# Performance work log

Hardware: AMD Instinct MI355X
Metric: run time of the kernel (lower is better)

The kernel has to match this reference:

```python
import jax, jax.numpy as jnp
import numpy as np

B, T, S, D, V, NX = 4, 256, 400, 512, 50000, 50
VEXT = V + NX  # extended vocab


def setup_inputs() -> dict:
    key = jax.random.key(0)
    ks = jax.random.split(key, 10)
    s = 0.02
    return {
        "x": jax.random.normal(ks[0], (B, T, D), dtype=jnp.float32),
        "enc_outputs": jax.random.normal(ks[1], (B, S, D), dtype=jnp.float32),
        "src_mask": jax.random.randint(ks[2], (B, 1, S), 0, 2, dtype=jnp.int32),
        "enc_batch_extend_vocab": jax.random.randint(ks[3], (B, S), 0, VEXT, dtype=jnp.int64),
        "extra_zeros": jnp.zeros((B, T, NX), dtype=jnp.float32),
        "fc_w": jax.random.normal(ks[4], (V, D), dtype=jnp.float32) * s,
        "fc_b": jnp.zeros((V,), dtype=jnp.float32),
        "pgen_w": jax.random.normal(ks[5], (1, D), dtype=jnp.float32) * s,
        "pgen_b": jnp.zeros((1,), dtype=jnp.float32),
        "wq": jax.random.normal(ks[6], (D, D), dtype=jnp.float32) * s,
        "bq": jnp.zeros((D,), dtype=jnp.float32),
        "wk": jax.random.normal(ks[7], (D, D), dtype=jnp.float32) * s,
        "bk": jnp.zeros((D,), dtype=jnp.float32),
    }


def reference(x, enc_outputs, src_mask, enc_batch_extend_vocab, extra_zeros,
              fc_w, fc_b, pgen_w, pgen_b, wq, bq, wk, bk):
    # vocab distribution: [B,T,V]
    p_vocab = jax.nn.softmax(x @ fc_w.T + fc_b, axis=-1)
    # single-head cross attention probs (h=1 -> d_k = D)
    q = x @ wq.T + bq                 # [B,T,D]
    k = enc_outputs @ wk.T + bk       # [B,S,D]
    scores = jnp.einsum('btd,bsd->bts', q, k) / jnp.sqrt(jnp.float32(D))
    scores = jnp.where(src_mask == 0, jnp.float32(-1e9), scores)  # mask [B,1,S]
    attn_probs = jax.nn.softmax(scores, axis=-1)  # [B,T,S]
    # generation gate
    p_gen = jax.nn.sigmoid(x @ pgen_w.T + pgen_b)  # [B,T,1]
    attn_dist = (1.0 - p_gen) * attn_probs         # copy distribution over source
    p_ext = jnp.concatenate([p_gen * p_vocab, extra_zeros], axis=-1)  # [B,T,VEXT]
    # scatter-add copy probs into extended vocab slots
    b_idx = jnp.arange(B)[:, None, None]
    t_idx = jnp.arange(T)[None, :, None]
    v_idx = enc_batch_extend_vocab[:, None, :]
    bb, tt, vv = jnp.broadcast_arrays(b_idx, t_idx, v_idx)  # each [B,T,S]
    p_ext = p_ext.at[bb, tt, vv].add(attn_dist)
    return jnp.log(jnp.maximum(p_ext, jnp.float32(1e-9)))
```

## Files before the change

kernel.cpp:

```cpp
#include <hip/hip_runtime.h>
#include <hip/hip_bf16.h>
#include <math.h>

constexpr int cB = 4, cT = 256, cS = 400, cD = 512, cV = 50000, cNX = 50;
constexpr int cVEXT = cV + cNX;
constexpr int cPAN  = (cV + 127) / 128;
constexpr int cCBLD = cVEXT * 2;

typedef __attribute__((ext_vector_type(8))) short short8v;
typedef __attribute__((ext_vector_type(4))) float floatx4;

__device__ inline ushort f2bf(float f) {
    union { float f; unsigned u; } v; v.f = f;
    unsigned r = (v.u + 0x7FFFu + ((v.u >> 16) & 1u)) >> 16;
    return (ushort)r;
}
__device__ inline float bf2f(ushort u) {
    union { unsigned u; float f; } v; v.u = ((unsigned)u) << 16;
    return v.f;
}

__global__ __launch_bounds__(256) void cast_kernel(
    const float* __restrict__ src, ushort* __restrict__ dst, int n4)
{
    const int stride = gridDim.x * 256;
    for (int i = blockIdx.x * 256 + threadIdx.x; i < n4; i += stride) {
        float4 v = *(const float4*)(src + (size_t)i * 4);
        ushort4 o;
        o.x = f2bf(v.x); o.y = f2bf(v.y); o.z = f2bf(v.z); o.w = f2bf(v.w);
        *(ushort4*)(dst + (size_t)i * 4) = o;
    }
}

template<bool STATS>
__global__ __launch_bounds__(256) void gemm2(
    const ushort* __restrict__ A, const ushort* __restrict__ Wb,
    const float* __restrict__ bias,
    float* __restrict__ Cf, ushort* __restrict__ Cb,
    float* __restrict__ pm, float* __restrict__ ps,
    int M, int N, int K, int ldc)
{
    __shared__ ushort As[2][128 * 32];
    __shared__ ushort Bs[2][128 * 32];
    __shared__ float sm_m[2][128];
    __shared__ float sm_s[2][128];

    const int tid  = threadIdx.x;
    const int lane = tid & 63;
    const int wv   = tid >> 6;
    const int wm   = wv >> 1;
    const int wn   = wv & 1;
    const int bm   = blockIdx.x * 128;
    const int bn   = blockIdx.y * 128;

    const int srow = lane >> 2;
    const int sk   = (lane & 3) * 8;

    const int nt = K >> 5;

    floatx4 acc[4][4] = {};

    auto stage = [&](int bidx, int t) {
        const int k0 = t * 32;
        #pragma unroll
        for (int c = 0; c < 2; ++c) {
            const int lr = wv * 32 + c * 16;
            int ga = bm + lr + srow; if (ga >= M) ga = M - 1;
            __builtin_amdgcn_global_load_lds(
                (const __attribute__((address_space(1))) void*)(A + (size_t)ga * K + k0 + sk),
                (__attribute__((address_space(3))) void*)&As[bidx][lr * 32], 16, 0, 0);
        }
        #pragma unroll
        for (int c = 0; c < 2; ++c) {
            const int lr = wv * 32 + c * 16;
            int gb = bn + lr + srow; if (gb >= N) gb = N - 1;
            __builtin_amdgcn_global_load_lds(
                (const __attribute__((address_space(1))) void*)(Wb + (size_t)gb * K + k0 + sk),
                (__attribute__((address_space(3))) void*)&Bs[bidx][lr * 32], 16, 0, 0);
        }
    };

    stage(0, 0);
    __syncthreads();

    const int fr = lane & 15;
    const int g  = lane >> 4;
    int buf = 0;

    for (int t = 0; t < nt; ++t) {
        if (t + 1 < nt) stage(buf ^ 1, t + 1);
        short8v a[4], b[4];
        #pragma unroll
        for (int mi = 0; mi < 4; ++mi)
            a[mi] = *(const short8v*)&As[buf][(wm * 64 + mi * 16 + fr) * 32 + g * 8];
        #pragma unroll
        for (int ni = 0; ni < 4; ++ni)
            b[ni] = *(const short8v*)&Bs[buf][(wn * 64 + ni * 16 + fr) * 32 + g * 8];
        #pragma unroll
        for (int mi = 0; mi < 4; ++mi)
            #pragma unroll
            for (int ni = 0; ni < 4; ++ni)
                acc[mi][ni] = __builtin_amdgcn_mfma_f32_16x16x32_bf16(
                    a[mi], b[ni], acc[mi][ni], 0, 0, 0);
        __syncthreads();
        buf ^= 1;
    }

    float bv[4]; bool val[4];
    #pragma unroll
    for (int ni = 0; ni < 4; ++ni) {
        const int colg = bn + wn * 64 + ni * 16 + fr;
        val[ni] = (colg < N);
        bv[ni] = val[ni] ? bias[colg] : 0.f;
    }
    #pragma unroll
    for (int mi = 0; mi < 4; ++mi)
        #pragma unroll
        for (int ni = 0; ni < 4; ++ni)
            #pragma unroll
            for (int r = 0; r < 4; ++r)
                acc[mi][ni][r] += bv[ni];

    if constexpr (STATS) {
        #pragma unroll
        for (int mi = 0; mi < 4; ++mi) {
            #pragma unroll
            for (int r = 0; r < 4; ++r) {
                float mx = -1e30f;
                #pragma unroll
                for (int ni = 0; ni < 4; ++ni)
                    if (val[ni]) mx = fmaxf(mx, acc[mi][ni][r]);
                #pragma unroll
                for (int sw = 1; sw < 16; sw <<= 1)
                    mx = fmaxf(mx, __shfl_xor(mx, sw));
                float sm = 0.f;
                #pragma unroll
                for (int ni = 0; ni < 4; ++ni)
                    if (val[ni]) sm += __expf(acc[mi][ni][r] - mx);
                #pragma unroll
                for (int sw = 1; sw < 16; sw <<= 1)
                    sm += __shfl_xor(sm, sw);
                if (fr == 0) {
                    const int rl = wm * 64 + mi * 16 + g * 4 + r;
                    sm_m[wn][rl] = mx;
                    sm_s[wn][rl] = sm;
                }
            }
        }
        __syncthreads();
        if (tid < 128) {
            const float m0 = sm_m[0][tid], m1 = sm_m[1][tid];
            const float s0 = sm_s[0][tid], s1 = sm_s[1][tid];
            const float mm = fmaxf(m0, m1);
            const float ss = s0 * __expf(m0 - mm) + s1 * __expf(m1 - mm);
            const int grow = bm + tid;
            if (grow < M) {
                pm[(size_t)grow * cPAN + blockIdx.y] = mm;
                ps[(size_t)grow * cPAN + blockIdx.y] = ss;
            }
        }
        #pragma unroll
        for (int mi = 0; mi < 4; ++mi) {
            #pragma unroll
            for (int ni = 0; ni < 4; ++ni) {
                if (!val[ni]) continue;
                const int colg = bn + wn * 64 + ni * 16 + fr;
                #pragma unroll
                for (int r = 0; r < 4; ++r) {
                    const int row = bm + wm * 64 + mi * 16 + g * 4 + r;
                    if (row < M) Cb[(size_t)row * cCBLD + colg] = f2bf(acc[mi][ni][r]);
                }
            }
        }
    } else {
        #pragma unroll
        for (int mi = 0; mi < 4; ++mi) {
            #pragma unroll
            for (int ni = 0; ni < 4; ++ni) {
                if (!val[ni]) continue;
                const int colg = bn + wn * 64 + ni * 16 + fr;
                #pragma unroll
                for (int r = 0; r < 4; ++r) {
                    const int row = bm + wm * 64 + mi * 16 + g * 4 + r;
                    if (row < M) Cf[(size_t)row * ldc + colg] = acc[mi][ni][r];
                }
            }
        }
    }
}

__global__ __launch_bounds__(256) void combine_kernel(
    const float* __restrict__ pm, const float* __restrict__ ps,
    const float* __restrict__ pgen, float* __restrict__ rowadd)
{
    const int row = blockIdx.x;
    const int tid = threadIdx.x;
    float m = -1e30f, s = 0.f;
    for (int i = tid; i < cPAN; i += 256) {
        const float mi = pm[(size_t)row * cPAN + i];
        const float si = ps[(size_t)row * cPAN + i];
        const float nm = fmaxf(m, mi);
        s = s * __expf(m - nm) + si * __expf(mi - nm);
        m = nm;
    }
    #pragma unroll
    for (int sw = 1; sw < 64; sw <<= 1) {
        const float mo = __shfl_xor(m, sw);
        const float so = __shfl_xor(s, sw);
        const float nm = fmaxf(m, mo);
        s = s * __expf(m - nm) + so * __expf(mo - nm);
        m = nm;
    }
    __shared__ float rm[4], rs[4];
    if ((tid & 63) == 0) { rm[tid >> 6] = m; rs[tid >> 6] = s; }
    __syncthreads();
    if (tid == 0) {
        m = rm[0]; s = rs[0];
        #pragma unroll
        for (int i = 1; i < 4; ++i) {
            const float nm = fmaxf(m, rm[i]);
            s = s * __expf(m - nm) + rs[i] * __expf(rm[i] - nm);
            m = nm;
        }
        rowadd[row] = __logf(pgen[row]) - m - __logf(s);
    }
}

__global__ __launch_bounds__(512) void transform_inplace(
    float* __restrict__ out, const float* __restrict__ rowadd,
    const int* __restrict__ ebev, const float* __restrict__ attn)
{
    const int row = blockIdx.x;
    const int b   = row / cT;
    const int tid = threadIdx.x;
    constexpr float LOGMIN = -20.72326583694641f;

    __shared__ int   pos[cS];
    __shared__ float add[cS];
    for (int s = tid; s < cS; s += 512) {
        pos[s] = ebev[b * cS + s];
        add[s] = attn[(size_t)row * cS + s];
    }

    const float a = rowadd[row];
    ushort* rowu = (ushort*)out + (size_t)row * cCBLD;
    float*  rowf = out + (size_t)row * cVEXT;

    #pragma unroll 1
    for (int L = 32768; L >= 2; L >>= 1) {
        const int hi = (2 * L < cVEXT) ? 2 * L : cVEXT;
        for (int i = L + 2 * tid; i < hi; i += 1024) {
            const float x0 = bf2f(rowu[i]);
            const float x1 = bf2f(rowu[i + 1]);
            float2 o;
            o.x = (i     < cV) ? fmaxf(x0 + a, LOGMIN) : LOGMIN;
            o.y = (i + 1 < cV) ? fmaxf(x1 + a, LOGMIN) : LOGMIN;
            *(float2*)&rowf[i] = o;
        }
        __syncthreads();
    }
    if (tid == 0) {
        const float x1 = bf2f(rowu[1]);
        const float x0 = bf2f(rowu[0]);
        rowf[1] = fmaxf(x1 + a, LOGMIN);
        rowf[0] = fmaxf(x0 + a, LOGMIN);
    }
    __syncthreads();

    for (int s = tid; s < cS; s += 512) {
        const int p = pos[s];
        bool leader = true;
        for (int s2 = 0; s2 < s; ++s2)
            if (pos[s2] == p) { leader = false; break; }
        if (!leader) continue;
        float sum = add[s];
        for (int s2 = s + 1; s2 < cS; ++s2)
            if (pos[s2] == p) sum += add[s2];
        const float base = __expf(rowf[p]);
        rowf[p] = __logf(fmaxf(base + sum, 1e-9f));
    }
}

__global__ __launch_bounds__(64) void pgen_kernel(
    const float* __restrict__ x, const float* __restrict__ w,
    const float* __restrict__ b, float* __restrict__ pgen)
{
    const int row = blockIdx.x;
    const int lane = threadIdx.x;
    const float* xr = x + (size_t)row * cD;
    float s = 0.f;
    for (int i = lane; i < cD; i += 64) s += xr[i] * w[i];
    #pragma unroll
    for (int off = 32; off; off >>= 1) s += __shfl_down(s, off);
    if (lane == 0) pgen[row] = 1.f / (1.f + __expf(-(s + b[0])));
}

__global__ __launch_bounds__(256) void attn_kernel(
    const float* __restrict__ q, const float* __restrict__ k,
    const int* __restrict__ src_mask, const float* __restrict__ pgen,
    float* __restrict__ attn)
{
    constexpr float scale = 0.04419417382415922f;
    const int row = blockIdx.x;
    const int b = row / cT;
    const int tid = threadIdx.x;

    __shared__ __align__(16) float qs[cD];
    __shared__ float sc[cS];
    __shared__ float red[4];

    for (int i = tid; i < cD; i += 256) qs[i] = q[(size_t)row * cD + i];
    __syncthreads();

    for (int s = tid; s < cS; s += 256) {
        const float* kr = k + ((size_t)b * cS + s) * cD;
        float dot = 0.f;
        #pragma unroll 4
        for (int i = 0; i < cD; i += 4) {
            float4 kv = *(const float4*)(kr + i);
            float4 qv = *(const float4*)(qs + i);
            dot += qv.x * kv.x + qv.y * kv.y + qv.z * kv.z + qv.w * kv.w;
        }
        float v = dot * scale;
        if (src_mask[b * cS + s] == 0) v = -1e9f;
        sc[s] = v;
    }
    __syncthreads();

    float m = -3.4e38f;
    for (int s = tid; s < cS; s += 256) m = fmaxf(m, sc[s]);
    #pragma unroll
    for (int off = 32; off; off >>= 1) m = fmaxf(m, __shfl_down(m, off));
    if ((tid & 63) == 0) red[tid >> 6] = m;
    __syncthreads();
    m = fmaxf(fmaxf(red[0], red[1]), fmaxf(red[2], red[3]));
    __syncthreads();

    float sum = 0.f;
    for (int s = tid; s < cS; s += 256) {
        float e = __expf(sc[s] - m);
        sc[s] = e;
        sum += e;
    }
    #pragma unroll
    for (int off = 32; off; off >>= 1) sum += __shfl_down(sum, off);
    if ((tid & 63) == 0) red[tid >> 6] = sum;
    __syncthreads();
    sum = red[0] + red[1] + red[2] + red[3];

    const float w = (1.f - pgen[row]) / sum;
    for (int s = tid; s < cS; s += 256)
        attn[(size_t)row * cS + s] = sc[s] * w;
}

extern "C" void kernel_launch(void* const* d_in, const int* in_sizes, int n_in,
                              void* d_out, int out_size, void* d_ws, size_t ws_size,
                              hipStream_t stream)
{
    const float* x      = (const float*)d_in[0];
    const float* enc    = (const float*)d_in[1];
    const int*   mask   = (const int*)d_in[2];
    const int*   ebev   = (const int*)d_in[3];
    const float* fc_w   = (const float*)d_in[5];
    const float* fc_b   = (const float*)d_in[6];
    const float* pgen_w = (const float*)d_in[7];
    const float* pgen_b = (const float*)d_in[8];
    const float* wq     = (const float*)d_in[9];
    const float* bq     = (const float*)d_in[10];
    const float* wk     = (const float*)d_in[11];
    const float* bk     = (const float*)d_in[12];
    float* out = (float*)d_out;

    float* ws     = (float*)d_ws;
    float* q      = ws;
    float* kbuf   = q + (size_t)cB * cT * cD;
    float* pgen   = kbuf + (size_t)cB * cS * cD;
    float* attn   = pgen + cB * cT;
    float* pm     = attn + (size_t)cB * cT * cS;
    float* ps     = pm + (size_t)cB * cT * cPAN;
    float* rowadd = ps + (size_t)cB * cT * cPAN;
    ushort* xb    = (ushort*)(rowadd + cB * cT);
    ushort* encb  = xb + (size_t)cB * cT * cD;
    ushort* wqb   = encb + (size_t)cB * cS * cD;
    ushort* wkb   = wqb + (size_t)cD * cD;
    ushort* wb    = wkb + (size_t)cD * cD;

    const dim3 blk(256);
    const int MQ = cB * cT;
    const int MK = cB * cS;

    cast_kernel<<<dim3(512), blk, 0, stream>>>(x, xb, (cB * cT * cD) / 4);
    cast_kernel<<<dim3(512), blk, 0, stream>>>(enc, encb, (cB * cS * cD) / 4);
    cast_kernel<<<dim3(256), blk, 0, stream>>>(wq, wqb, (cD * cD) / 4);
    cast_kernel<<<dim3(256), blk, 0, stream>>>(wk, wkb, (cD * cD) / 4);
    cast_kernel<<<dim3(2048), blk, 0, stream>>>(fc_w, wb, (cV * cD) / 4);

    gemm2<false><<<dim3(MQ / 128, cD / 128), blk, 0, stream>>>(
        xb, wqb, bq, q, nullptr, nullptr, nullptr, MQ, cD, cD, cD);
    gemm2<false><<<dim3((MK + 127) / 128, cD / 128), blk, 0, stream>>>(
        encb, wkb, bk, kbuf, nullptr, nullptr, nullptr, MK, cD, cD, cD);
    pgen_kernel<<<dim3(MQ), dim3(64), 0, stream>>>(x, pgen_w, pgen_b, pgen);

    attn_kernel<<<dim3(MQ), blk, 0, stream>>>(q, kbuf, mask, pgen, attn);

    gemm2<true><<<dim3(MQ / 128, cPAN), blk, 0, stream>>>(
        xb, wb, fc_b, nullptr, (ushort*)out, pm, ps, MQ, cV, cD, 0);

    combine_kernel<<<dim3(MQ), blk, 0, stream>>>(pm, ps, pgen, rowadd);

    transform_inplace<<<dim3(MQ), dim3(512), 0, stream>>>(
        out, rowadd, ebev, attn);
}
```

Measured before the change: 413.4 us.

## Stage bf16 logits in workspace, add flat transform plus scatter fixup, remap vocab GEMM tiles

When the workspace is large enough, the bf16 vocab logits are written to a separate workspace buffer and the bf16 weight copy is placed in the output buffer. A grid-parallel flat transform then writes log-probs without in-place aliasing, and a separate fixup kernel applies the copy-distribution scatter-add per unique source token. The vocab GEMM also remaps workgroup IDs so that blocks sharing a weight panel are grouped together, and it stores panel stats transposed for coalesced writes. The aim is more parallel, coalesced final-transform traffic and better weight-panel locality. The cost is an extra kernel launch and an O(S^2) duplicate scan per row in the fixup.

```diff
diff --git a/kernel.cpp b/kernel.cpp
--- a/kernel.cpp
+++ b/kernel.cpp
@@ -6,6 +6,7 @@
 constexpr int cVEXT = cV + cNX;
 constexpr int cPAN  = (cV + 127) / 128;
 constexpr int cCBLD = cVEXT * 2;
+constexpr int cMQ   = cB * cT;
 
 typedef __attribute__((ext_vector_type(8))) short short8v;
 typedef __attribute__((ext_vector_type(4))) float floatx4;
@@ -36,7 +37,7 @@
 __global__ __launch_bounds__(256) void gemm2(
     const ushort* __restrict__ A, const ushort* __restrict__ Wb,
     const float* __restrict__ bias,
-    float* __restrict__ Cf, ushort* __restrict__ Cb,
+    float* __restrict__ Cf, ushort* __restrict__ Cb, int cbld,
     float* __restrict__ pm, float* __restrict__ ps,
     int M, int N, int K, int ldc)
 {
@@ -50,8 +51,19 @@
     const int wv   = tid >> 6;
     const int wm   = wv >> 1;
     const int wn   = wv & 1;
-    const int bm   = blockIdx.x * 128;
-    const int bn   = blockIdx.y * 128;
+
+    int bm, bn, pan = 0;
+    if constexpr (STATS) {
+        const int wg  = blockIdx.y * gridDim.x + blockIdx.x;
+        const int nwg = gridDim.x * gridDim.y;
+        const int j   = (wg & 7) * (nwg >> 3) + (wg >> 3);
+        pan = j >> 3;
+        bm  = (j & 7) * 128;
+        bn  = pan * 128;
+    } else {
+        bm = blockIdx.x * 128;
+        bn = blockIdx.y * 128;
+    }
 
     const int srow = lane >> 2;
     const int sk   = (lane & 3) * 8;
@@ -155,8 +167,8 @@
             const float ss = s0 * __expf(m0 - mm) + s1 * __expf(m1 - mm);
             const int grow = bm + tid;
             if (grow < M) {
-                pm[(size_t)grow * cPAN + blockIdx.y] = mm;
-                ps[(size_t)grow * cPAN + blockIdx.y] = ss;
+                pm[(size_t)pan * M + grow] = mm;
+                ps[(size_t)pan * M + grow] = ss;
             }
         }
         #pragma unroll
@@ -168,7 +180,7 @@
                 #pragma unroll
                 for (int r = 0; r < 4; ++r) {
                     const int row = bm + wm * 64 + mi * 16 + g * 4 + r;
-                    if (row < M) Cb[(size_t)row * cCBLD + colg] = f2bf(acc[mi][ni][r]);
+                    if (row < M) Cb[(size_t)row * cbld + colg] = f2bf(acc[mi][ni][r]);
                 }
             }
         }
@@ -197,8 +209,8 @@
     const int tid = threadIdx.x;
     float m = -1e30f, s = 0.f;
     for (int i = tid; i < cPAN; i += 256) {
-        const float mi = pm[(size_t)row * cPAN + i];
-        const float si = ps[(size_t)row * cPAN + i];
+        const float mi = pm[(size_t)i * cMQ + row];
+        const float si = ps[(size_t)i * cMQ + row];
         const float nm = fmaxf(m, mi);
         s = s * __expf(m - nm) + si * __expf(mi - nm);
         m = nm;
@@ -223,6 +235,66 @@
             m = nm;
         }
         rowadd[row] = __logf(pgen[row]) - m - __logf(s);
+    }
+}
+
+__global__ __launch_bounds__(512) void transform_flat(
+    float* __restrict__ out, const ushort* __restrict__ lb,
+    const float* __restrict__ rowadd)
+{
+    const int row = blockIdx.y;
+    const float a = rowadd[row];
+    constexpr float LOGMIN = -20.72326583694641f;
+    const ushort* src = lb + (size_t)row * cV;
+    float* dst = out + (size_t)row * cVEXT;
+    constexpr int NI = cV / 8;
+    for (int i = blockIdx.x * 512 + threadIdx.x; i <= NI; i += gridDim.x * 512) {
+        if (i < NI) {
+            const short8v sv = *(const short8v*)(src + (size_t)i * 8);
+            const int v = i * 8;
+            #pragma unroll
+            for (int j = 0; j < 4; ++j) {
+                float2 o;
+                o.x = fmaxf(bf2f((ushort)sv[2 * j])     + a, LOGMIN);
+                o.y = fmaxf(bf2f((ushort)sv[2 * j + 1]) + a, LOGMIN);
+                *(float2*)&dst[v + 2 * j] = o;
+            }
+        } else {
+            #pragma unroll
+            for (int v = cV; v < cVEXT; v += 2) {
+                float2 o; o.x = LOGMIN; o.y = LOGMIN;
+                *(float2*)&dst[v] = o;
+            }
+        }
+    }
+}
+
+__global__ __launch_bounds__(256) void fixup_kernel(
+    float* __restrict__ out, const int* __restrict__ ebev,
+    const float* __restrict__ attn)
+{
+    const int row = blockIdx.x;
+    const int b = row / cT;
+    const int tid = threadIdx.x;
+    __shared__ int   pos[cS];
+    __shared__ float add[cS];
+    for (int s = tid; s < cS; s += 256) {
+        pos[s] = ebev[b * cS + s];
+        add[s] = attn[(size_t)row * cS + s];
+    }
+    __syncthreads();
+    float* rowf = out + (size_t)row * cVEXT;
+    for (int s = tid; s < cS; s += 256) {
+        const int p = pos[s];
+        bool leader = true;
+        for (int s2 = 0; s2 < s; ++s2)
+            if (pos[s2] == p) { leader = false; break; }
+        if (!leader) continue;
+        float sum = add[s];
+        for (int s2 = s + 1; s2 < cS; ++s2)
+            if (pos[s2] == p) sum += add[s2];
+        const float base = __expf(rowf[p]);
+        rowf[p] = __logf(fmaxf(base + sum, 1e-9f));
     }
 }
 
@@ -377,17 +449,33 @@
     float* pgen   = kbuf + (size_t)cB * cS * cD;
     float* attn   = pgen + cB * cT;
     float* pm     = attn + (size_t)cB * cT * cS;
-    float* ps     = pm + (size_t)cB * cT * cPAN;
-    float* rowadd = ps + (size_t)cB * cT * cPAN;
-    ushort* xb    = (ushort*)(rowadd + cB * cT);
+    float* ps     = pm + (size_t)cPAN * cMQ;
+    float* rowadd = ps + (size_t)cPAN * cMQ;
+    ushort* xb    = (ushort*)(rowadd + cMQ);
     ushort* encb  = xb + (size_t)cB * cT * cD;
     ushort* wqb   = encb + (size_t)cB * cS * cD;
     ushort* wkb   = wqb + (size_t)cD * cD;
-    ushort* wb    = wkb + (size_t)cD * cD;
+    ushort* tail  = wkb + (size_t)cD * cD;
+
+    const size_t base_bytes = (size_t)((char*)tail - (char*)d_ws);
+    const bool big = ws_size >= base_bytes + (size_t)cMQ * cV * 2 + 1024;
 
     const dim3 blk(256);
-    const int MQ = cB * cT;
+    const int MQ = cMQ;
     const int MK = cB * cS;
+
+    ushort* wb;
+    ushort* logitsb;
+    int     cbld;
+    if (big) {
+        wb = (ushort*)d_out;
+        logitsb = tail;
+        cbld = cV;
+    } else {
+        wb = tail;
+        logitsb = (ushort*)d_out;
+        cbld = cCBLD;
+    }
 
     cast_kernel<<<dim3(512), blk, 0, stream>>>(x, xb, (cB * cT * cD) / 4);
     cast_kernel<<<dim3(512), blk, 0, stream>>>(enc, encb, (cB * cS * cD) / 4);
@@ -396,18 +484,22 @@
     cast_kernel<<<dim3(2048), blk, 0, stream>>>(fc_w, wb, (cV * cD) / 4);
 
     gemm2<false><<<dim3(MQ / 128, cD / 128), blk, 0, stream>>>(
-        xb, wqb, bq, q, nullptr, nullptr, nullptr, MQ, cD, cD, cD);
+        xb, wqb, bq, q, nullptr, 0, nullptr, nullptr, MQ, cD, cD, cD);
     gemm2<false><<<dim3((MK + 127) / 128, cD / 128), blk, 0, stream>>>(
-        encb, wkb, bk, kbuf, nullptr, nullptr, nullptr, MK, cD, cD, cD);
+        encb, wkb, bk, kbuf, nullptr, 0, nullptr, nullptr, MK, cD, cD, cD);
     pgen_kernel<<<dim3(MQ), dim3(64), 0, stream>>>(x, pgen_w, pgen_b, pgen);
 
     attn_kernel<<<dim3(MQ), blk, 0, stream>>>(q, kbuf, mask, pgen, attn);
 
     gemm2<true><<<dim3(MQ / 128, cPAN), blk, 0, stream>>>(
-        xb, wb, fc_b, nullptr, (ushort*)out, pm, ps, MQ, cV, cD, 0);
+        xb, wb, fc_b, nullptr, logitsb, cbld, pm, ps, MQ, cV, cD, 0);
 
     combine_kernel<<<dim3(MQ), blk, 0, stream>>>(pm, ps, pgen, rowadd);
 
-    transform_inplace<<<dim3(MQ), dim3(512), 0, stream>>>(
-        out, rowadd, ebev, attn);
-}
+    if (big) {
+        transform_flat<<<dim3(13, MQ), dim3(512), 0, stream>>>(out, logitsb, rowadd);
+        fixup_kernel<<<dim3(MQ), blk, 0, stream>>>(out, ebev, attn);
+    } else {
+        transform_inplace<<<dim3(MQ), dim3(512), 0, stream>>>(out, rowadd, ebev, attn);
+    }
+}
```

Result: slower. 455.7 us (+10.2%).
